# Kernel optimization log

Measured on AMD Instinct MI355X. Metric: run time of the kernel, lower is better.

Reference implementation:

```python
import jax, jax.numpy as jnp
import numpy as np
from jax import lax

B, CIN, COUT, H, W = 4, 32, 64, 192, 192
K = 3  # kernel size
RED = 16  # SE reduction
EPS = 1e-5


def _conv2d_same(x, w, b):
    y = lax.conv_general_dilated(x, w, (1, 1), 'SAME',
                                 dimension_numbers=('NCHW', 'OIHW', 'NCHW'))
    return y + b[None, :, None, None]


def _bilinear_gather(x, py, px):
    # x: [B,C,H,W]; py/px: [B,KK,H,W] absolute sample coords -> [B,C,KK,H,W]
    Bb, C, Hh, Ww = x.shape
    KK = py.shape[1]
    y0 = jnp.floor(py); x0 = jnp.floor(px)
    wy = py - y0; wx = px - x0
    x_flat = x.reshape(Bb, C, Hh * Ww)

    def corner(yi, xi, wgt):
        valid = (yi >= 0) & (yi < Hh) & (xi >= 0) & (xi < Ww)
        yc = jnp.clip(yi, 0, Hh - 1).astype(jnp.int32)
        xc = jnp.clip(xi, 0, Ww - 1).astype(jnp.int32)
        idx = (yc * Ww + xc).reshape(Bb, 1, KK * Hh * Ww)
        g = jnp.take_along_axis(x_flat, idx, axis=2).reshape(Bb, C, KK, Hh, Ww)
        w_eff = (wgt * valid.astype(x.dtype))[:, None]  # [B,1,KK,H,W]
        return g * w_eff

    out = (corner(y0, x0, (1 - wy) * (1 - wx))
           + corner(y0, x0 + 1, (1 - wy) * wx)
           + corner(y0 + 1, x0, wy * (1 - wx))
           + corner(y0 + 1, x0 + 1, wy * wx))
    return out  # [B,C,KK,H,W]


def _deform_conv(x, offsets, w, b):
    # torchvision DeformConv2d, stride 1, pad 1, dilation 1, 1 offset group.
    Bb, C, Hh, Ww = x.shape
    off = offsets.reshape(Bb, K * K, 2, Hh, Ww)
    dy, dx = off[:, :, 0], off[:, :, 1]  # [B,KK,H,W]
    ky, kx = jnp.meshgrid(jnp.arange(K) - 1, jnp.arange(K) - 1, indexing='ij')
    hg, wg = jnp.meshgrid(jnp.arange(Hh), jnp.arange(Ww), indexing='ij')
    py = hg[None, None] + ky.reshape(-1)[None, :, None, None] + dy
    px = wg[None, None] + kx.reshape(-1)[None, :, None, None] + dx
    sampled = _bilinear_gather(x, py, px)  # [B,CIN,KK,H,W]
    y = jnp.einsum('bckhw,ock->bohw', sampled, w.reshape(w.shape[0], C, K * K))
    return y + b[None, :, None, None]


def _forward(x, w_off, b_off, w_def, b_def, bn_gamma, bn_beta,
             fc1_w, fc1_b, fc2_w, fc2_b):
    offsets = _conv2d_same(x, w_off, b_off)
    y = _deform_conv(x, offsets, w_def, b_def)
    # BatchNorm2d (training-mode batch statistics)
    mean = jnp.mean(y, axis=(0, 2, 3), keepdims=True)
    var = jnp.var(y, axis=(0, 2, 3), keepdims=True)
    y = (y - mean) * lax.rsqrt(var + EPS)
    y = y * bn_gamma[None, :, None, None] + bn_beta[None, :, None, None]
    # SE layer
    s = jnp.mean(y, axis=(2, 3))  # [B,C]
    s = jax.nn.relu(s @ fc1_w.T + fc1_b)
    s = jax.nn.sigmoid(s @ fc2_w.T + fc2_b)
    y = y * s[:, :, None, None]
    y = jax.nn.relu(y)
    # MaxPool 2x2 stride 2
    y = lax.reduce_window(y, -jnp.inf, lax.max, (1, 1, 2, 2), (1, 1, 2, 2), 'VALID')
    return y


def setup_inputs() -> dict:
    key = jax.random.key(0)
    ks = jax.random.split(key, 12)
    rn = lambda k, s, sc=1.0: (jax.random.normal(k, s, dtype=jnp.float32) * sc)
    return {
        'x': rn(ks[0], (B, CIN, H, W)),
        'w_off': rn(ks[1], (2 * K * K, CIN, K, K), 0.02),
        'b_off': jnp.zeros((2 * K * K,), jnp.float32),
        'w_def': rn(ks[2], (COUT, CIN, K, K), 0.05),
        'b_def': rn(ks[3], (COUT,), 0.05),
        'bn_gamma': jnp.ones((COUT,), jnp.float32),
        'bn_beta': jnp.zeros((COUT,), jnp.float32),
        'fc1_w': rn(ks[4], (COUT // RED, COUT), 0.1),
        'fc1_b': jnp.zeros((COUT // RED,), jnp.float32),
        'fc2_w': rn(ks[5], (COUT, COUT // RED), 0.1),
        'fc2_b': jnp.zeros((COUT,), jnp.float32),
    }


def reference(x, w_off, b_off, w_def, b_def, bn_gamma, bn_beta,
              fc1_w, fc1_b, fc2_w, fc2_b):
    return _forward(x, w_off, b_off, w_def, b_def, bn_gamma, bn_beta,
                    fc1_w, fc1_b, fc2_w, fc2_b)
```

## Files before the change

kernel.cpp:

```cpp
#include <hip/hip_runtime.h>
#include <math.h>

#define B_    4
#define CIN_  32
#define COUT_ 64
#define H_    192
#define W_    192
#define HW_   (H_ * W_)
#define NPIX_ (B_ * HW_)
#define EPS_  1e-5f

static __device__ __forceinline__ int swz1152(int blk) {
    return ((blk & 7) * 144) + (blk >> 3);
}

struct Cr { int o00, o01, o10, o11; float w00, w01, w10, w11; };

__global__ __launch_bounds__(256) void k_pre(
    const float* __restrict__ x, const float* __restrict__ w_def,
    const float* __restrict__ w_off, float* __restrict__ xt,
    float* __restrict__ wt_def, float* __restrict__ wt_off,
    float* __restrict__ stats)
{
    if (blockIdx.x < NPIX_ / 256) {
        const int pid = blockIdx.x * 256 + threadIdx.x;
        const int b   = pid / HW_;
        const int rem = pid - b * HW_;
        const float* xb = x + (size_t)b * CIN_ * HW_ + rem;
        float4 v[8];
#pragma unroll
        for (int j = 0; j < 8; ++j) {
            v[j].x = xb[(j * 4 + 0) * HW_];
            v[j].y = xb[(j * 4 + 1) * HW_];
            v[j].z = xb[(j * 4 + 2) * HW_];
            v[j].w = xb[(j * 4 + 3) * HW_];
        }
        float4* dst = (float4*)(xt + (size_t)pid * 32);
#pragma unroll
        for (int j = 0; j < 8; ++j) dst[j] = v[j];
    } else {
        const int i = (blockIdx.x - NPIX_ / 256) * 256 + threadIdx.x;
        if (i < 18432) {
            const int o  = i & 63;
            const int c  = (i >> 6) & 31;
            const int kk = i >> 11;
            wt_def[i] = w_def[(o * 32 + c) * 9 + kk];
        } else if (i < 18432 + 5760) {
            const int e  = i - 18432;
            const int o  = e % 20;
            const int t  = e / 20;
            const int c  = t & 31;
            const int kk = t >> 5;
            wt_off[e] = (o < 18) ? w_off[(o * 32 + c) * 9 + kk] : 0.f;
        } else if (i < 18432 + 5760 + 512) {
            stats[i - 18432 - 5760] = 0.f;
        }
    }
}

__global__ __launch_bounds__(512, 6) void k_conv_off(
    const float* __restrict__ xt, const float* __restrict__ wt,
    const float* __restrict__ b_off, float* __restrict__ offs)
{
    __shared__ float rlds[4 * 128 * 21];
    const int tid = threadIdx.x;
    const int px  = tid & 127;
    const int grp = __builtin_amdgcn_readfirstlane(tid >> 7);
    const int pid = swz1152(blockIdx.x) * 128 + px;
    const int b   = pid / HW_;
    const int rem = pid - b * HW_;
    const int h   = rem / W_;
    const int w   = rem - h * W_;
    const float* xg = xt + (size_t)b * HW_ * 32 + grp * 8;

    float acc[20];
#pragma unroll
    for (int o = 0; o < 20; ++o) acc[o] = 0.f;

    auto tapoff = [&](int kk, float& g) -> int {
        const int yy = h + kk / 3 - 1;
        const int sx = w + kk % 3 - 1;
        const bool ok = (yy >= 0) & (yy < H_) & (sx >= 0) & (sx < W_);
        g = ok ? 1.f : 0.f;
        const int cy = min(max(yy, 0), H_ - 1);
        const int cx = min(max(sx, 0), W_ - 1);
        return (cy * W_ + cx) * 32;
    };

    float g; int off = tapoff(0, g);
    float4 x0 = *(const float4*)(xg + off);
    float4 x1 = *(const float4*)(xg + off + 4);

#pragma unroll 1
    for (int kk = 0; kk < 9; ++kk) {
        float ng = 0.f; float4 nx0, nx1;
        if (kk < 8) {
            const int noff = tapoff(kk + 1, ng);
            nx0 = *(const float4*)(xg + noff);
            nx1 = *(const float4*)(xg + noff + 4);
        }
        const float vs[8] = {x0.x * g, x0.y * g, x0.z * g, x0.w * g,
                             x1.x * g, x1.y * g, x1.z * g, x1.w * g};
#pragma unroll
        for (int e = 0; e < 8; ++e) {
            const float4* wr = (const float4*)(wt + (kk * 32 + grp * 8 + e) * 20);
            const float a = vs[e];
#pragma unroll
            for (int q = 0; q < 5; ++q) {
                float4 wv = wr[q];
                acc[q * 4 + 0] += a * wv.x;
                acc[q * 4 + 1] += a * wv.y;
                acc[q * 4 + 2] += a * wv.z;
                acc[q * 4 + 3] += a * wv.w;
            }
        }
        x0 = nx0; x1 = nx1; g = ng;
    }

    float* rp = &rlds[(grp * 128 + px) * 21];
#pragma unroll
    for (int o = 0; o < 20; ++o) rp[o] = acc[o];
    __syncthreads();

#pragma unroll
    for (int j = 0; j < 5; ++j) {
        const int o = grp * 5 + j;
        if (o < 18) {
            const float s = rlds[(0 * 128 + px) * 21 + o]
                          + rlds[(1 * 128 + px) * 21 + o]
                          + rlds[(2 * 128 + px) * 21 + o]
                          + rlds[(3 * 128 + px) * 21 + o];
            offs[(b * 18 + o) * HW_ + rem] = s + b_off[o];
        }
    }
}

__global__ __launch_bounds__(512, 6) void k_deform(
    const float* __restrict__ xt, const float* __restrict__ offs,
    const float* __restrict__ wt, const float* __restrict__ b_def,
    float* __restrict__ y, float* __restrict__ sum_bc,
    float* __restrict__ sumsq_bc)
{
    __shared__ float vlds[32 * 128];
    const int tid  = threadIdx.x;
    const int px   = tid & 127;
    const int grp  = __builtin_amdgcn_readfirstlane(tid >> 7);
    const int lane = tid & 63;
    const int pid  = swz1152(blockIdx.x) * 128 + px;
    const int b    = pid / HW_;
    const int rem  = pid - b * HW_;
    const int h    = rem / W_;
    const int w    = rem - h * W_;
    const float* xg = xt + (size_t)b * HW_ * 32 + grp * 8;
    const float* ob = offs + b * 18 * HW_ + rem;

    float acc[16];
#pragma unroll
    for (int q = 0; q < 16; ++q) acc[q] = 0.f;

    auto mk = [&](int kk, float dy, float dx) -> Cr {
        const float py = (float)(h + kk / 3 - 1) + dy;
        const float qx = (float)(w + kk % 3 - 1) + dx;
        const float y0f = floorf(py), x0f = floorf(qx);
        const float wy = py - y0f, wx = qx - x0f;
        const int iy0 = (int)y0f, ix0 = (int)x0f;
        const int iy1 = iy0 + 1,  ix1 = ix0 + 1;
        const float vy0 = (iy0 >= 0 && iy0 < H_) ? 1.f : 0.f;
        const float vy1 = (iy1 >= 0 && iy1 < H_) ? 1.f : 0.f;
        const float vx0 = (ix0 >= 0 && ix0 < W_) ? 1.f : 0.f;
        const float vx1 = (ix1 >= 0 && ix1 < W_) ? 1.f : 0.f;
        Cr c;
        c.w00 = (1.f - wy) * (1.f - wx) * vy0 * vx0;
        c.w01 = (1.f - wy) * wx * vy0 * vx1;
        c.w10 = wy * (1.f - wx) * vy1 * vx0;
        c.w11 = wy * wx * vy1 * vx1;
        const int cy0 = min(max(iy0, 0), H_ - 1), cy1 = min(max(iy1, 0), H_ - 1);
        const int cx0 = min(max(ix0, 0), W_ - 1), cx1 = min(max(ix1, 0), W_ - 1);
        c.o00 = (cy0 * W_ + cx0) * 32; c.o01 = (cy0 * W_ + cx1) * 32;
        c.o10 = (cy1 * W_ + cx0) * 32; c.o11 = (cy1 * W_ + cx1) * 32;
        return c;
    };

    float dy = ob[0], dx = ob[HW_];
    Cr cur = mk(0, dy, dx);
    float4 A0 = *(const float4*)(xg + cur.o00), A1 = *(const float4*)(xg + cur.o00 + 4);
    float4 B0 = *(const float4*)(xg + cur.o01), B1 = *(const float4*)(xg + cur.o01 + 4);
    float4 C0 = *(const float4*)(xg + cur.o10), C1 = *(const float4*)(xg + cur.o10 + 4);
    float4 D0 = *(const float4*)(xg + cur.o11), D1 = *(const float4*)(xg + cur.o11 + 4);
    float ndy = ob[2 * HW_], ndx = ob[3 * HW_];

#pragma unroll 1
    for (int kk = 0; kk < 9; ++kk) {
        __syncthreads();
        float v[8];
        v[0] = cur.w00 * A0.x + cur.w01 * B0.x + cur.w10 * C0.x + cur.w11 * D0.x;
        v[1] = cur.w00 * A0.y + cur.w01 * B0.y + cur.w10 * C0.y + cur.w11 * D0.y;
        v[2] = cur.w00 * A0.z + cur.w01 * B0.z + cur.w10 * C0.z + cur.w11 * D0.z;
        v[3] = cur.w00 * A0.w + cur.w01 * B0.w + cur.w10 * C0.w + cur.w11 * D0.w;
        v[4] = cur.w00 * A1.x + cur.w01 * B1.x + cur.w10 * C1.x + cur.w11 * D1.x;
        v[5] = cur.w00 * A1.y + cur.w01 * B1.y + cur.w10 * C1.y + cur.w11 * D1.y;
        v[6] = cur.w00 * A1.z + cur.w01 * B1.z + cur.w10 * C1.z + cur.w11 * D1.z;
        v[7] = cur.w00 * A1.w + cur.w01 * B1.w + cur.w10 * C1.w + cur.w11 * D1.w;
#pragma unroll
        for (int j = 0; j < 8; ++j) vlds[(grp * 8 + j) * 128 + px] = v[j];

        if (kk < 8) {
            cur = mk(kk + 1, ndy, ndx);
            A0 = *(const float4*)(xg + cur.o00); A1 = *(const float4*)(xg + cur.o00 + 4);
            B0 = *(const float4*)(xg + cur.o01); B1 = *(const float4*)(xg + cur.o01 + 4);
            C0 = *(const float4*)(xg + cur.o10); C1 = *(const float4*)(xg + cur.o10 + 4);
            D0 = *(const float4*)(xg + cur.o11); D1 = *(const float4*)(xg + cur.o11 + 4);
            if (kk < 7) {
                ndy = ob[(2 * kk + 4) * HW_];
                ndx = ob[(2 * kk + 5) * HW_];
            }
        }
        __syncthreads();

        const float* wk = wt + (kk << 11) + (grp << 4);
#pragma unroll 8
        for (int c = 0; c < 32; ++c) {
            const float vv = vlds[c * 128 + px];
            const float4* wr = (const float4*)(wk + (c << 6));
            const float4 w0 = wr[0], w1 = wr[1], w2 = wr[2], w3 = wr[3];
            acc[ 0] += vv * w0.x; acc[ 1] += vv * w0.y;
            acc[ 2] += vv * w0.z; acc[ 3] += vv * w0.w;
            acc[ 4] += vv * w1.x; acc[ 5] += vv * w1.y;
            acc[ 6] += vv * w1.z; acc[ 7] += vv * w1.w;
            acc[ 8] += vv * w2.x; acc[ 9] += vv * w2.y;
            acc[10] += vv * w2.z; acc[11] += vv * w2.w;
            acc[12] += vv * w3.x; acc[13] += vv * w3.y;
            acc[14] += vv * w3.z; acc[15] += vv * w3.w;
        }
    }

    float* yp = y + ((size_t)b * COUT_ + grp * 16) * HW_ + rem;
#pragma unroll
    for (int q = 0; q < 16; ++q) {
        acc[q] += b_def[grp * 16 + q];
        yp[q * HW_] = acc[q];
    }

    float ls = 0.f, lq = 0.f;
#pragma unroll
    for (int o = 0; o < 16; ++o) {
        float t = acc[o];
        float u = t * t;
#pragma unroll
        for (int s = 32; s; s >>= 1) {
            t += __shfl_xor(t, s, 64);
            u += __shfl_xor(u, s, 64);
        }
        if (lane == o) { ls = t; lq = u; }
    }
    if (lane < 16) {
        atomicAdd(&sum_bc[b * 64 + grp * 16 + lane], ls);
        atomicAdd(&sumsq_bc[b * 64 + grp * 16 + lane], lq);
    }
}

__global__ __launch_bounds__(256) void k_finish(
    const float* __restrict__ y,
    const float* __restrict__ sum_bc, const float* __restrict__ sumsq_bc,
    const float* __restrict__ gamma, const float* __restrict__ beta,
    const float* __restrict__ fc1_w, const float* __restrict__ fc1_b,
    const float* __restrict__ fc2_w, const float* __restrict__ fc2_b,
    float* __restrict__ out)
{
    __shared__ float sal[256], sbb[256], sin_[256];
    const int tid = threadIdx.x;
    {
        const int b = tid >> 6, c = tid & 63;
        float ch_s = 0.f, ch_q = 0.f;
#pragma unroll
        for (int bb = 0; bb < 4; ++bb) {
            ch_s += sum_bc[bb * 64 + c];
            ch_q += sumsq_bc[bb * 64 + c];
        }
        const float invN = 1.f / (float)(B_ * HW_);
        const float mean = ch_s * invN;
        const float var  = ch_q * invN - mean * mean;
        const float a    = gamma[c] * rsqrtf(var + EPS_);
        const float bi   = beta[c] - mean * a;
        sin_[tid] = a * (sum_bc[tid] * (1.f / (float)HW_)) + bi;
        __syncthreads();
        float hv[4];
#pragma unroll
        for (int j = 0; j < 4; ++j) {
            float hs = fc1_b[j];
            for (int cc = 0; cc < 64; ++cc)
                hs += sin_[b * 64 + cc] * fc1_w[j * 64 + cc];
            hv[j] = fmaxf(hs, 0.f);
        }
        float o = fc2_b[c];
#pragma unroll
        for (int j = 0; j < 4; ++j) o += hv[j] * fc2_w[c * 4 + j];
        const float s = 1.f / (1.f + expf(-o));
        sal[tid] = a * s;
        sbb[tid] = bi * s;
    }
    __syncthreads();

    const int t    = blockIdx.x * 256 + tid;
    const int opix = t * 2;
    const int bc   = opix / (96 * 96);
    const int rem  = opix - bc * (96 * 96);
    const int oh   = rem / 96, ow = rem - oh * 96;
    const float al = sal[bc], bb = sbb[bc];
    const float* yp = y + (size_t)bc * HW_ + (2 * oh) * W_ + 2 * ow;
    const float4 r0 = *(const float4*)yp;
    const float4 r1 = *(const float4*)(yp + W_);
    float2 st;
    st.x = fmaxf(fmaxf(fmaxf(fmaf(r0.x, al, bb), fmaf(r0.y, al, bb)),
                       fmaxf(fmaf(r1.x, al, bb), fmaf(r1.y, al, bb))), 0.f);
    st.y = fmaxf(fmaxf(fmaxf(fmaf(r0.z, al, bb), fmaf(r0.w, al, bb)),
                       fmaxf(fmaf(r1.z, al, bb), fmaf(r1.w, al, bb))), 0.f);
    *(float2*)(out + opix) = st;
}

extern "C" void kernel_launch(void* const* d_in, const int* in_sizes, int n_in,
                              void* d_out, int out_size, void* d_ws, size_t ws_size,
                              hipStream_t stream)
{
    const float* x     = (const float*)d_in[0];
    const float* w_off = (const float*)d_in[1];
    const float* b_off = (const float*)d_in[2];
    const float* w_def = (const float*)d_in[3];
    const float* b_def = (const float*)d_in[4];
    const float* gamma = (const float*)d_in[5];
    const float* beta  = (const float*)d_in[6];
    const float* fc1_w = (const float*)d_in[7];
    const float* fc1_b = (const float*)d_in[8];
    const float* fc2_w = (const float*)d_in[9];
    const float* fc2_b = (const float*)d_in[10];
    float* out = (float*)d_out;

    float* ws   = (float*)d_ws;
    float* offs   = ws;
    float* yb     = offs + 2654208;
    float* xt     = yb + 9437184;
    float* wt_def = xt + 4718592;
    float* wt_off = wt_def + 18432;
    float* stats  = wt_off + 5760;
    float* sum_bc   = stats;
    float* sumsq_bc = stats + 256;

    k_pre     <<<dim3(NPIX_ / 256 + 97), dim3(256), 0, stream>>>(
                  x, w_def, w_off, xt, wt_def, wt_off, stats);
    k_conv_off<<<dim3(NPIX_ / 128), dim3(512), 0, stream>>>(xt, wt_off, b_off, offs);
    k_deform  <<<dim3(NPIX_ / 128), dim3(512), 0, stream>>>(xt, offs, wt_def, b_def,
                                                            yb, sum_bc, sumsq_bc);
    k_finish  <<<dim3(B_ * COUT_ * 96 * 96 / 512), dim3(256), 0, stream>>>(
                  yb, sum_bc, sumsq_bc, gamma, beta,
                  fc1_w, fc1_b, fc2_w, fc2_b, out);
}
```

Baseline: 248.9 us.

## Remap gather threads so four lanes share a pixel for coalesced channel loads

In both the offset conv and deform kernels, the gather phase now gives each pixel four consecutive threads covering its 32 channels (tid&3 selects the channel group), instead of spreading one pixel's channel groups across separate 128-thread groups. Adjacent lanes therefore read contiguous channel-last memory, which should coalesce the scattered bilinear corner loads. The matmul phase keeps the old pixel-per-thread mapping, and LDS is relaid as pixel-major rows padded to 36 floats so it can be written and read with float4. The cost is a thread remap through LDS, possible bank conflicts with the new stride, and less spatial locality per wavefront across pixels.

Measured after the change: 633.9 us. 155% more time.

```diff
diff --git a/kernel.cpp b/kernel.cpp
--- a/kernel.cpp
+++ b/kernel.cpp
@@ -62,16 +62,20 @@
     const float* __restrict__ xt, const float* __restrict__ wt,
     const float* __restrict__ b_off, float* __restrict__ offs)
 {
-    __shared__ float rlds[4 * 128 * 21];
+    __shared__ float rlds[512 * 21];
     const int tid = threadIdx.x;
-    const int px  = tid & 127;
-    const int grp = __builtin_amdgcn_readfirstlane(tid >> 7);
-    const int pid = swz1152(blockIdx.x) * 128 + px;
-    const int b   = pid / HW_;
-    const int rem = pid - b * HW_;
-    const int h   = rem / W_;
-    const int w   = rem - h * W_;
-    const float* xg = xt + (size_t)b * HW_ * 32 + grp * 8;
+    const int px1 = tid >> 2;
+    const int g1  = tid & 3;
+    const int px2 = tid & 127;
+    const int jg  = __builtin_amdgcn_readfirstlane(tid >> 7);
+
+    const int base = swz1152(blockIdx.x) * 128;
+    const int b    = base / HW_;
+    const int rb   = base - b * HW_;
+    const int rem1 = rb + px1;
+    const int h    = rem1 / W_;
+    const int w    = rem1 - h * W_;
+    const float* xg = xt + (size_t)b * HW_ * 32 + g1 * 8;
 
     float acc[20];
 #pragma unroll
@@ -103,7 +107,7 @@
                              x1.x * g, x1.y * g, x1.z * g, x1.w * g};
 #pragma unroll
         for (int e = 0; e < 8; ++e) {
-            const float4* wr = (const float4*)(wt + (kk * 32 + grp * 8 + e) * 20);
+            const float4* wr = (const float4*)(wt + (kk * 32 + g1 * 8 + e) * 20);
             const float a = vs[e];
 #pragma unroll
             for (int q = 0; q < 5; ++q) {
@@ -117,20 +121,21 @@
         x0 = nx0; x1 = nx1; g = ng;
     }
 
-    float* rp = &rlds[(grp * 128 + px) * 21];
+    float* rp = &rlds[(px1 * 4 + g1) * 21];
 #pragma unroll
     for (int o = 0; o < 20; ++o) rp[o] = acc[o];
     __syncthreads();
 
+    const int rem2 = rb + px2;
 #pragma unroll
     for (int j = 0; j < 5; ++j) {
-        const int o = grp * 5 + j;
+        const int o = jg * 5 + j;
         if (o < 18) {
-            const float s = rlds[(0 * 128 + px) * 21 + o]
-                          + rlds[(1 * 128 + px) * 21 + o]
-                          + rlds[(2 * 128 + px) * 21 + o]
-                          + rlds[(3 * 128 + px) * 21 + o];
-            offs[(b * 18 + o) * HW_ + rem] = s + b_off[o];
+            const float s = rlds[(px2 * 4 + 0) * 21 + o]
+                          + rlds[(px2 * 4 + 1) * 21 + o]
+                          + rlds[(px2 * 4 + 2) * 21 + o]
+                          + rlds[(px2 * 4 + 3) * 21 + o];
+            offs[(b * 18 + o) * HW_ + rem2] = s + b_off[o];
         }
     }
 }
@@ -141,18 +146,22 @@
     float* __restrict__ y, float* __restrict__ sum_bc,
     float* __restrict__ sumsq_bc)
 {
-    __shared__ float vlds[32 * 128];
+    __shared__ float vlds[128 * 36];
     const int tid  = threadIdx.x;
-    const int px   = tid & 127;
-    const int grp  = __builtin_amdgcn_readfirstlane(tid >> 7);
+    const int px1  = tid >> 2;
+    const int g1   = tid & 3;
+    const int px2  = tid & 127;
+    const int og   = __builtin_amdgcn_readfirstlane(tid >> 7);
     const int lane = tid & 63;
-    const int pid  = swz1152(blockIdx.x) * 128 + px;
-    const int b    = pid / HW_;
-    const int rem  = pid - b * HW_;
-    const int h    = rem / W_;
-    const int w    = rem - h * W_;
-    const float* xg = xt + (size_t)b * HW_ * 32 + grp * 8;
-    const float* ob = offs + b * 18 * HW_ + rem;
+
+    const int base = swz1152(blockIdx.x) * 128;
+    const int b    = base / HW_;
+    const int rb   = base - b * HW_;
+    const int rem1 = rb + px1;
+    const int h    = rem1 / W_;
+    const int w    = rem1 - h * W_;
+    const float* xg = xt + (size_t)b * HW_ * 32 + g1 * 8;
+    const float* ob = offs + b * 18 * HW_ + rem1;
 
     float acc[16];
 #pragma unroll
@@ -192,17 +201,17 @@
 #pragma unroll 1
     for (int kk = 0; kk < 9; ++kk) {
         __syncthreads();
-        float v[8];
-        v[0] = cur.w00 * A0.x + cur.w01 * B0.x + cur.w10 * C0.x + cur.w11 * D0.x;
-        v[1] = cur.w00 * A0.y + cur.w01 * B0.y + cur.w10 * C0.y + cur.w11 * D0.y;
-        v[2] = cur.w00 * A0.z + cur.w01 * B0.z + cur.w10 * C0.z + cur.w11 * D0.z;
-        v[3] = cur.w00 * A0.w + cur.w01 * B0.w + cur.w10 * C0.w + cur.w11 * D0.w;
-        v[4] = cur.w00 * A1.x + cur.w01 * B1.x + cur.w10 * C1.x + cur.w11 * D1.x;
-        v[5] = cur.w00 * A1.y + cur.w01 * B1.y + cur.w10 * C1.y + cur.w11 * D1.y;
-        v[6] = cur.w00 * A1.z + cur.w01 * B1.z + cur.w10 * C1.z + cur.w11 * D1.z;
-        v[7] = cur.w00 * A1.w + cur.w01 * B1.w + cur.w10 * C1.w + cur.w11 * D1.w;
-#pragma unroll
-        for (int j = 0; j < 8; ++j) vlds[(grp * 8 + j) * 128 + px] = v[j];
+        float4 v0, v1;
+        v0.x = cur.w00 * A0.x + cur.w01 * B0.x + cur.w10 * C0.x + cur.w11 * D0.x;
+        v0.y = cur.w00 * A0.y + cur.w01 * B0.y + cur.w10 * C0.y + cur.w11 * D0.y;
+        v0.z = cur.w00 * A0.z + cur.w01 * B0.z + cur.w10 * C0.z + cur.w11 * D0.z;
+        v0.w = cur.w00 * A0.w + cur.w01 * B0.w + cur.w10 * C0.w + cur.w11 * D0.w;
+        v1.x = cur.w00 * A1.x + cur.w01 * B1.x + cur.w10 * C1.x + cur.w11 * D1.x;
+        v1.y = cur.w00 * A1.y + cur.w01 * B1.y + cur.w10 * C1.y + cur.w11 * D1.y;
+        v1.z = cur.w00 * A1.z + cur.w01 * B1.z + cur.w10 * C1.z + cur.w11 * D1.z;
+        v1.w = cur.w00 * A1.w + cur.w01 * B1.w + cur.w10 * C1.w + cur.w11 * D1.w;
+        *(float4*)&vlds[px1 * 36 + g1 * 8]     = v0;
+        *(float4*)&vlds[px1 * 36 + g1 * 8 + 4] = v1;
 
         if (kk < 8) {
             cur = mk(kk + 1, ndy, ndx);
@@ -217,27 +226,34 @@
         }
         __syncthreads();
 
-        const float* wk = wt + (kk << 11) + (grp << 4);
-#pragma unroll 8
-        for (int c = 0; c < 32; ++c) {
-            const float vv = vlds[c * 128 + px];
-            const float4* wr = (const float4*)(wk + (c << 6));
-            const float4 w0 = wr[0], w1 = wr[1], w2 = wr[2], w3 = wr[3];
-            acc[ 0] += vv * w0.x; acc[ 1] += vv * w0.y;
-            acc[ 2] += vv * w0.z; acc[ 3] += vv * w0.w;
-            acc[ 4] += vv * w1.x; acc[ 5] += vv * w1.y;
-            acc[ 6] += vv * w1.z; acc[ 7] += vv * w1.w;
-            acc[ 8] += vv * w2.x; acc[ 9] += vv * w2.y;
-            acc[10] += vv * w2.z; acc[11] += vv * w2.w;
-            acc[12] += vv * w3.x; acc[13] += vv * w3.y;
-            acc[14] += vv * w3.z; acc[15] += vv * w3.w;
-        }
-    }
-
-    float* yp = y + ((size_t)b * COUT_ + grp * 16) * HW_ + rem;
+        const float* wk = wt + (kk << 11) + (og << 4);
+        const float* vp = &vlds[px2 * 36];
+#pragma unroll
+        for (int j = 0; j < 8; ++j) {
+            const float4 vv = *(const float4*)(vp + 4 * j);
+            const float vs[4] = {vv.x, vv.y, vv.z, vv.w};
+#pragma unroll
+            for (int e = 0; e < 4; ++e) {
+                const float4* wr = (const float4*)(wk + ((j * 4 + e) << 6));
+                const float4 w0 = wr[0], w1 = wr[1], w2 = wr[2], w3 = wr[3];
+                const float vc = vs[e];
+                acc[ 0] += vc * w0.x; acc[ 1] += vc * w0.y;
+                acc[ 2] += vc * w0.z; acc[ 3] += vc * w0.w;
+                acc[ 4] += vc * w1.x; acc[ 5] += vc * w1.y;
+                acc[ 6] += vc * w1.z; acc[ 7] += vc * w1.w;
+                acc[ 8] += vc * w2.x; acc[ 9] += vc * w2.y;
+                acc[10] += vc * w2.z; acc[11] += vc * w2.w;
+                acc[12] += vc * w3.x; acc[13] += vc * w3.y;
+                acc[14] += vc * w3.z; acc[15] += vc * w3.w;
+            }
+        }
+    }
+
+    const int rem2 = rb + px2;
+    float* yp = y + ((size_t)b * COUT_ + og * 16) * HW_ + rem2;
 #pragma unroll
     for (int q = 0; q < 16; ++q) {
-        acc[q] += b_def[grp * 16 + q];
+        acc[q] += b_def[og * 16 + q];
         yp[q * HW_] = acc[q];
     }
 
@@ -254,8 +270,8 @@
         if (lane == o) { ls = t; lq = u; }
     }
     if (lane < 16) {
-        atomicAdd(&sum_bc[b * 64 + grp * 16 + lane], ls);
-        atomicAdd(&sumsq_bc[b * 64 + grp * 16 + lane], lq);
+        atomicAdd(&sum_bc[b * 64 + og * 16 + lane], ls);
+        atomicAdd(&sumsq_bc[b * 64 + og * 16 + lane], lq);
     }
 }
 
```
